# Optimization experiments

Hardware: AMD Instinct MI355X
Metric: run time of the kernel (lower is better)

## Reference

```python
import jax, jax.numpy as jnp
import numpy as np

N = 150000   # total supergraph nodes (entities+events+chains)
D = 128      # embed_size
H = 4        # attention heads
DH = D // H  # head dim
E = 300000   # edges per layer
L = 4        # layer_specs length
A = 8        # edge attr dim
T = 10       # num_edge_type
TIME_SCALE = 24.0
SLOPE = 0.2  # negative_slope


def setup_inputs() -> dict:
    key = jax.random.key(0)
    ks = jax.random.split(key, 16)
    nrm = lambda k, s, sc=1.0: jax.random.normal(k, s, dtype=jnp.float32) * sc
    return {
        'x': nrm(ks[0], (N, D), 0.1),
        'Wq': nrm(ks[1], (L, D, D), D ** -0.5),
        'Wk': nrm(ks[2], (L, D, D), D ** -0.5),
        'Wv': nrm(ks[3], (L, D, D), D ** -0.5),
        'Wskip': nrm(ks[4], (L, D, D), D ** -0.5),
        'Wa': nrm(ks[5], (L, A, D), 0.1),
        'time_w': nrm(ks[6], (D,)),
        'time_b': nrm(ks[7], (D,), 0.1),
        'dist_w': nrm(ks[8], (D,)),
        'dist_b': nrm(ks[9], (D,), 0.1),
        'type_table': nrm(ks[10], (T, D), 0.1),
        'bn_gamma': jnp.ones((L, D), jnp.float32),
        'bn_beta': jnp.zeros((L, D), jnp.float32),
        'beta': jnp.full((L,), 0.5, jnp.float32),
        'edge_attr': jax.random.uniform(ks[11], (L, E, A), dtype=jnp.float32),
        'edge_dt': jax.random.uniform(ks[12], (L, E), dtype=jnp.float32) * TIME_SCALE,
        'edge_ds': jax.random.uniform(ks[13], (L, E), dtype=jnp.float32) * 10.0,
        'edge_index': jax.random.randint(ks[14], (L, 2, E), 0, N),
        'edge_type': jax.random.randint(ks[15], (L, E), 0, T),
    }


def _layer(x, Wq, Wk, Wv, Wskip, Wa, time_w, time_b, dist_w, dist_b,
           type_table, gamma, bvec, beta, attr, dt, ds, ei, et):
    n = x.shape[0]
    src, dst = ei[0], ei[1]
    # continuous time / distance encoders: cos basis (TimeEncoder / 'time' DistanceEncoder)
    te = jnp.cos((dt / TIME_SCALE)[:, None] * time_w + time_b)   # [E,D]
    de = jnp.cos(ds[:, None] * dist_w + dist_b)                  # [E,D]
    # 'add' edge/time fusion: attr MLP + time + dist + edge-type embeddings
    edge_feat = attr @ Wa + te + de + type_table[et]             # [E,D]
    kv_in = x[src] + edge_feat                                   # gather + fuse
    q = (x @ Wq).reshape(n, H, DH)[dst]                          # [E,H,DH]
    k = (kv_in @ Wk).reshape(-1, H, DH)
    v = (kv_in @ Wv).reshape(-1, H, DH)
    logits = (q * k).sum(-1) * (DH ** -0.5)                      # [E,H]
    logits = jnp.where(logits >= 0, logits, SLOPE * logits)      # leaky_relu(negative_slope)
    # segment softmax over incoming edges of each destination node
    m = jax.ops.segment_max(logits, dst, num_segments=n)
    a = jnp.exp(logits - m[dst])
    denom = jax.ops.segment_sum(a, dst, num_segments=n)
    a = a / denom[dst]
    agg = jax.ops.segment_sum(a[..., None] * v, dst, num_segments=n).reshape(n, D)
    # beta-weighted residual (learn_beta) with skip projection
    out = beta * (x @ Wskip) + (1.0 - beta) * agg
    # BatchNorm1d (training-mode batch stats) + ReLU
    mu = out.mean(0)
    var = out.var(0)
    out = (out - mu) * jax.lax.rsqrt(var + 1e-5) * gamma + bvec
    return jax.nn.relu(out)


def reference(x, Wq, Wk, Wv, Wskip, Wa, time_w, time_b, dist_w, dist_b,
              type_table, bn_gamma, bn_beta, beta, edge_attr, edge_dt,
              edge_ds, edge_index, edge_type):
    for l in range(L):  # entity2event, event2event, event2chain (time filter), chain2chain
        x = _layer(x, Wq[l], Wk[l], Wv[l], Wskip[l], Wa[l],
                   time_w, time_b, dist_w, dist_b, type_table,
                   bn_gamma[l], bn_beta[l], beta[l],
                   edge_attr[l], edge_dt[l], edge_ds[l],
                   edge_index[l], edge_type[l])
    return x
```

## Files before the change

### kernel.cpp

```cpp
#include <hip/hip_runtime.h>

typedef unsigned int u32;
typedef unsigned short u16;
typedef short bf16x8 __attribute__((ext_vector_type(8)));
typedef float f32x4 __attribute__((ext_vector_type(4)));

#define N_NODES 150000
#define E_EDGES 300000
#define L_CNT   151552
#define ETILES  9375
#define NTILES  4688

__device__ __forceinline__ float blo(u32 u){ return __uint_as_float(u << 16); }
__device__ __forceinline__ float bhi(u32 u){ return __uint_as_float(u & 0xffff0000u); }
__device__ __forceinline__ float b2f(u16 h){ return __uint_as_float(((u32)h) << 16); }
__device__ __forceinline__ u16 f2bf(float f){
  u32 u = __float_as_uint(f);
  return (u16)((u + 0x7fffu + ((u >> 16) & 1u)) >> 16);
}
__device__ __forceinline__ u32 pack2(float a, float b){
  return (u32)f2bf(a) | ((u32)f2bf(b) << 16);
}

__device__ __forceinline__ f32x4 mfma16(bf16x8 a, bf16x8 b, f32x4 c){
  return __builtin_amdgcn_mfma_f32_16x16x32_bf16(a, b, c, 0, 0, 0);
}

__device__ __forceinline__ int opsw(int r, int k){ return (r * 128 + k) ^ ((r & 7) << 3); }
__device__ __forceinline__ int csw(int r, int n){ return (r * 128 + n) ^ (((r >> 2) & 3) << 3); }

__global__ __launch_bounds__(256)
void k_wt(const float* __restrict__ Wq, const float* __restrict__ Wk,
          const float* __restrict__ Wv, const float* __restrict__ Ws,
          u16* __restrict__ Wt)
{
  const int m = blockIdx.x;
  const float* src = (m < 4 ? Wq : m < 8 ? Wk : m < 12 ? Wv : Ws)
                     + (size_t)(m & 3) * 16384;
  u16* dst = Wt + (size_t)m * 16384;
  const int t = threadIdx.x;
  for (int i = 0; i < 16; ++i) {
    int idx = i * 256 + t;
    int n = idx >> 5;
    int k4 = (idx & 31) << 2;
    ushort4 o;
    o.x = f2bf(src[(k4 + 0) * 128 + n]);
    o.y = f2bf(src[(k4 + 1) * 128 + n]);
    o.z = f2bf(src[(k4 + 2) * 128 + n]);
    o.w = f2bf(src[(k4 + 3) * 128 + n]);
    *(ushort4*)(dst + n * 128 + k4) = o;
  }
}


__global__ __launch_bounds__(256)
void k_hist(const int* __restrict__ eidx, int* __restrict__ counts)
{
  const int l = blockIdx.y;
  const int e = blockIdx.x * 256 + threadIdx.x;
  if (e < E_EDGES) {
    int dst = eidx[(size_t)l * 2 * E_EDGES + E_EDGES + e];
    atomicAdd(&counts[(size_t)l * L_CNT + dst], 1);
  }
}

__global__ __launch_bounds__(256)
void k_scan1(const int* __restrict__ counts, int* __restrict__ rowptr,
             int* __restrict__ bsum)
{
  __shared__ int sh[256];
  const int b = blockIdx.x, l = blockIdx.y;
  const int t = threadIdx.x;
  const int* c = counts + (size_t)l * L_CNT + b * 2048;
  int* rp = rowptr + (size_t)l * L_CNT + b * 2048;
  int v[8]; int s = 0;
  #pragma unroll
  for (int j = 0; j < 8; ++j) { v[j] = c[t * 8 + j]; s += v[j]; }
  sh[t] = s; __syncthreads();
  for (int off = 1; off < 256; off <<= 1) {
    int x = (t >= off) ? sh[t - off] : 0;
    __syncthreads();
    sh[t] += x;
    __syncthreads();
  }
  int excl = (t == 0) ? 0 : sh[t - 1];
  if (t == 255) bsum[l * 128 + b] = sh[255];
  int run = excl;
  #pragma unroll
  for (int j = 0; j < 8; ++j) { rp[t * 8 + j] = run; run += v[j]; }
}

__global__ __launch_bounds__(128)
void k_scan2(int* __restrict__ bsum)
{
  __shared__ int sh[128];
  const int l = blockIdx.x, t = threadIdx.x;
  int v = (t < 74) ? bsum[l * 128 + t] : 0;
  sh[t] = v; __syncthreads();
  for (int off = 1; off < 128; off <<= 1) {
    int x = (t >= off) ? sh[t - off] : 0;
    __syncthreads();
    sh[t] += x;
    __syncthreads();
  }
  int excl = (t == 0) ? 0 : sh[t - 1];
  if (t < 74) bsum[l * 128 + t] = excl;
}

__global__ __launch_bounds__(256)
void k_scan3(int* __restrict__ rowptr, int* __restrict__ tmp,
             const int* __restrict__ bsum)
{
  const int l = blockIdx.y;
  const int q = blockIdx.x * 256 + threadIdx.x;
  int v = rowptr[(size_t)l * L_CNT + q] + bsum[l * 128 + (q >> 11)];
  rowptr[(size_t)l * L_CNT + q] = v;
  tmp[(size_t)l * L_CNT + q] = v;
}

__global__ __launch_bounds__(256)
void k_scatter(const int* __restrict__ srcP, const int* __restrict__ dstP,
               const int* __restrict__ etP, const float* __restrict__ dtP,
               const float* __restrict__ dsP, const float* __restrict__ attrP,
               int* __restrict__ tmpL, u32* __restrict__ meta)
{
  const int e = blockIdx.x * 256 + threadIdx.x;
  if (e < E_EDGES) {
    int dst = dstP[e];
    int pos = atomicAdd(&tmpL[dst], 1);
    int src = srcP[e];
    int et  = etP[e];
    float dtn = dtP[e] * (1.0f / 24.0f);
    float dsv = dsP[e];
    float4 aA = *(const float4*)(attrP + (size_t)e * 8);
    float4 aB = *(const float4*)(attrP + (size_t)e * 8 + 4);
    uint4 r0, r1;
    r0.x = (u32)src;
    r0.y = (u32)dst | ((u32)et << 20);
    r0.z = __float_as_uint(dtn);
    r0.w = __float_as_uint(dsv);
    r1.x = pack2(aA.x, aA.y); r1.y = pack2(aA.z, aA.w);
    r1.z = pack2(aB.x, aB.y); r1.w = pack2(aB.z, aB.w);
    u32* mp = meta + (size_t)pos * 8;
    *(uint4*)mp = r0;
    *(uint4*)(mp + 4) = r1;
  }
}

template<int XF32>
__global__ __launch_bounds__(256)
void k_kvin(const void* __restrict__ xg, const float* __restrict__ Wa,
            const float* __restrict__ tw, const float* __restrict__ tb,
            const float* __restrict__ dw, const float* __restrict__ db,
            const float* __restrict__ ttab, const u32* __restrict__ meta,
            u16* __restrict__ kvV)
{
  const int idx = blockIdx.x * 256 + threadIdx.x;
  const int e = idx >> 4;
  const int c8 = (idx & 15) << 3;
  const u32* mp = meta + (size_t)e * 8;
  uint4 m0 = *(const uint4*)mp;
  uint4 m1 = *(const uint4*)(mp + 4);
  const int src = (int)m0.x;
  const int et = (int)(m0.y >> 20);
  const float dtn = __uint_as_float(m0.z);
  const float dss = __uint_as_float(m0.w);
  float aa[8] = { blo(m1.x), bhi(m1.x), blo(m1.y), bhi(m1.y),
                  blo(m1.z), bhi(m1.z), blo(m1.w), bhi(m1.w) };
  const float4 twA = *(const float4*)(tw + c8);
  const float4 twB = *(const float4*)(tw + c8 + 4);
  const float4 tbA = *(const float4*)(tb + c8);
  const float4 tbB = *(const float4*)(tb + c8 + 4);
  const float4 dwA = *(const float4*)(dw + c8);
  const float4 dwB = *(const float4*)(dw + c8 + 4);
  const float4 dbA = *(const float4*)(db + c8);
  const float4 dbB = *(const float4*)(db + c8 + 4);
  const float4 ttA = *(const float4*)(ttab + et * 128 + c8);
  const float4 ttB = *(const float4*)(ttab + et * 128 + c8 + 4);
  float f[8];
  f[0] = __cosf(fmaf(dtn, twA.x, tbA.x)) + __cosf(fmaf(dss, dwA.x, dbA.x)) + ttA.x;
  f[1] = __cosf(fmaf(dtn, twA.y, tbA.y)) + __cosf(fmaf(dss, dwA.y, dbA.y)) + ttA.y;
  f[2] = __cosf(fmaf(dtn, twA.z, tbA.z)) + __cosf(fmaf(dss, dwA.z, dbA.z)) + ttA.z;
  f[3] = __cosf(fmaf(dtn, twA.w, tbA.w)) + __cosf(fmaf(dss, dwA.w, dbA.w)) + ttA.w;
  f[4] = __cosf(fmaf(dtn, twB.x, tbB.x)) + __cosf(fmaf(dss, dwB.x, dbB.x)) + ttB.x;
  f[5] = __cosf(fmaf(dtn, twB.y, tbB.y)) + __cosf(fmaf(dss, dwB.y, dbB.y)) + ttB.y;
  f[6] = __cosf(fmaf(dtn, twB.z, tbB.z)) + __cosf(fmaf(dss, dwB.z, dbB.z)) + ttB.z;
  f[7] = __cosf(fmaf(dtn, twB.w, tbB.w)) + __cosf(fmaf(dss, dwB.w, dbB.w)) + ttB.w;
  #pragma unroll
  for (int a = 0; a < 8; ++a) {
    float4 wA = *(const float4*)(Wa + a * 128 + c8);
    float4 wB = *(const float4*)(Wa + a * 128 + c8 + 4);
    f[0] = fmaf(aa[a], wA.x, f[0]);
    f[1] = fmaf(aa[a], wA.y, f[1]);
    f[2] = fmaf(aa[a], wA.z, f[2]);
    f[3] = fmaf(aa[a], wA.w, f[3]);
    f[4] = fmaf(aa[a], wB.x, f[4]);
    f[5] = fmaf(aa[a], wB.y, f[5]);
    f[6] = fmaf(aa[a], wB.z, f[6]);
    f[7] = fmaf(aa[a], wB.w, f[7]);
  }
  float xv[8];
  if (XF32) {
    float4 xA = *(const float4*)((const float*)xg + (size_t)src * 128 + c8);
    float4 xB = *(const float4*)((const float*)xg + (size_t)src * 128 + c8 + 4);
    xv[0] = xA.x; xv[1] = xA.y; xv[2] = xA.z; xv[3] = xA.w;
    xv[4] = xB.x; xv[5] = xB.y; xv[6] = xB.z; xv[7] = xB.w;
  } else {
    uint4 xr = *(const uint4*)((const u16*)xg + (size_t)src * 128 + c8);
    xv[0] = blo(xr.x); xv[1] = bhi(xr.x); xv[2] = blo(xr.y); xv[3] = bhi(xr.y);
    xv[4] = blo(xr.z); xv[5] = bhi(xr.z); xv[6] = blo(xr.w); xv[7] = bhi(xr.w);
  }
  uint4 o;
  o.x = pack2(xv[0] + f[0], xv[1] + f[1]);
  o.y = pack2(xv[2] + f[2], xv[3] + f[3]);
  o.z = pack2(xv[4] + f[4], xv[5] + f[5]);
  o.w = pack2(xv[6] + f[6], xv[7] + f[7]);
  *(uint4*)(kvV + (size_t)e * 128 + c8) = o;
}


template<int XF32>
__global__ __launch_bounds__(128, 2)
void gemm_qs(const void* __restrict__ xg, const u16* __restrict__ WtQ,
             const u16* __restrict__ WtS, u16* __restrict__ Qo,
             u16* __restrict__ So)
{
  __shared__ __align__(16) u16 As[4160];
  __shared__ __align__(16) u16 Bs[4160];
  const int t = threadIdx.x;
  const int w = t >> 6, lane = t & 63;
  const int lr = lane & 15, hi = lane >> 4;
  const int row0 = blockIdx.x * 32;
  const int nr = min(32, N_NODES - row0);
  const u16* Wt = w ? WtS : WtQ;
  u16* C = w ? So : Qo;

  bf16x8 wt[8][4];
  #pragma unroll
  for (int nb = 0; nb < 8; ++nb)
    #pragma unroll
    for (int ks = 0; ks < 4; ++ks)
      wt[nb][ks] = *(const bf16x8*)(Wt + (nb * 16 + lr) * 128 + ks * 32 + hi * 8);

  #pragma unroll
  for (int i = 0; i < 4; ++i) {
    int idx = i * 128 + t;
    int r = idx >> 4, c8 = (idx & 15) << 3;
    if (r < nr) {
      if (XF32) {
        float4 vA = *(const float4*)((const float*)xg + (size_t)(row0 + r) * 128 + c8);
        float4 vB = *(const float4*)((const float*)xg + (size_t)(row0 + r) * 128 + c8 + 4);
        uint4 o;
        o.x = pack2(vA.x, vA.y); o.y = pack2(vA.z, vA.w);
        o.z = pack2(vB.x, vB.y); o.w = pack2(vB.z, vB.w);
        *(uint4*)(As + opsw(r, c8)) = o;
      } else {
        uint4 v = *(const uint4*)((const u16*)xg + (size_t)(row0 + r) * 128 + c8);
        *(uint4*)(As + opsw(r, c8)) = v;
      }
    } else {
      *(uint4*)(As + opsw(r, c8)) = make_uint4(0, 0, 0, 0);
    }
  }
  __syncthreads();

  f32x4 acc[2][8];
  #pragma unroll
  for (int a = 0; a < 2; ++a)
    #pragma unroll
    for (int b = 0; b < 8; ++b) {
      acc[a][b][0] = 0.f; acc[a][b][1] = 0.f;
      acc[a][b][2] = 0.f; acc[a][b][3] = 0.f;
    }
  #pragma unroll
  for (int ks = 0; ks < 4; ++ks) {
    const int kb = ks * 32 + hi * 8;
    bf16x8 a0 = *(const bf16x8*)(As + opsw(lr, kb));
    bf16x8 a1 = *(const bf16x8*)(As + opsw(16 + lr, kb));
    #pragma unroll
    for (int nb = 0; nb < 8; ++nb) {
      acc[0][nb] = mfma16(a0, wt[nb][ks], acc[0][nb]);
      acc[1][nb] = mfma16(a1, wt[nb][ks], acc[1][nb]);
    }
  }
  __syncthreads();

  u16* Cs = w ? Bs : As;
  const int g4 = hi << 2;
  #pragma unroll
  for (int mt = 0; mt < 2; ++mt)
    #pragma unroll
    for (int nt = 0; nt < 8; ++nt)
      #pragma unroll
      for (int j = 0; j < 4; ++j)
        Cs[csw(mt * 16 + g4 + j, nt * 16 + lr)] = f2bf(acc[mt][nt][j]);
  #pragma unroll
  for (int i = 0; i < 8; ++i) {
    int idx = i * 64 + lane;
    int r = idx >> 4, n8 = (idx & 15) << 3;
    if (r < nr) {
      uint4 v = *(const uint4*)(Cs + csw(r, n8));
      *(uint4*)(C + (size_t)(row0 + r) * 128 + n8) = v;
    }
  }
}


__global__ __launch_bounds__(128, 2)
void edge_kv(const u16* __restrict__ WtK, const u16* __restrict__ WtV,
             const u32* __restrict__ meta, const u16* __restrict__ Qb,
             u16* __restrict__ kvV, float* __restrict__ logits)
{
  __shared__ __align__(16) u16 KVs[4160];
  __shared__ __align__(16) u16 Qs[4160];
  __shared__ int dstSh[32];
  const int t = threadIdx.x;
  const int w = t >> 6, lane = t & 63;
  const int lr = lane & 15, hi = lane >> 4;
  const int e0 = blockIdx.x * 32;
  const u16* Wt = w ? WtV : WtK;

  bf16x8 wt[8][4];
  #pragma unroll
  for (int nb = 0; nb < 8; ++nb)
    #pragma unroll
    for (int ks = 0; ks < 4; ++ks)
      wt[nb][ks] = *(const bf16x8*)(Wt + (nb * 16 + lr) * 128 + ks * 32 + hi * 8);

  if (w == 0) {
    #pragma unroll
    for (int i = 0; i < 8; ++i) {
      int idx = i * 64 + lane;
      int r = idx >> 4, c8 = (idx & 15) << 3;
      uint4 v = *(const uint4*)(kvV + (size_t)(e0 + r) * 128 + c8);
      *(uint4*)(KVs + opsw(r, c8)) = v;
    }
  } else {
    if (lane < 32)
      dstSh[lane] = (int)(meta[(size_t)(e0 + lane) * 8 + 1] & 0xFFFFFu);
    #pragma unroll
    for (int i = 0; i < 8; ++i) {
      int idx = i * 64 + lane;
      int r = idx >> 4, c8 = (idx & 15) << 3;
      int qrow = dstSh[r];
      uint4 qv = *(const uint4*)(Qb + (size_t)qrow * 128 + c8);
      *(uint4*)(Qs + opsw(r, c8)) = qv;
    }
  }
  __syncthreads();

  if (w == 0) {
    #pragma unroll
    for (int eb = 0; eb < 2; ++eb) {
      f32x4 kacc[8];
      #pragma unroll
      for (int b = 0; b < 8; ++b) {
        kacc[b][0] = 0.f; kacc[b][1] = 0.f; kacc[b][2] = 0.f; kacc[b][3] = 0.f;
      }
      #pragma unroll
      for (int ks = 0; ks < 4; ++ks) {
        bf16x8 ef = *(const bf16x8*)(KVs + opsw(eb * 16 + lr, ks * 32 + hi * 8));
        #pragma unroll
        for (int nb = 0; nb < 8; ++nb)
          kacc[nb] = mfma16(wt[nb][ks], ef, kacc[nb]);
      }
      const int el = eb * 16 + lr;
      float hs[4] = {0.f, 0.f, 0.f, 0.f};
      #pragma unroll
      for (int nb = 0; nb < 8; ++nb) {
        ushort4 q = *(const ushort4*)(Qs + opsw(el, nb * 16 + hi * 4));
        hs[nb >> 1] += b2f(q.x) * kacc[nb][0] + b2f(q.y) * kacc[nb][1]
                     + b2f(q.z) * kacc[nb][2] + b2f(q.w) * kacc[nb][3];
      }
      #pragma unroll
      for (int h = 0; h < 4; ++h) {
        hs[h] += __shfl_xor(hs[h], 16, 64);
        hs[h] += __shfl_xor(hs[h], 32, 64);
        hs[h] *= 0.17677669529663687f;
        hs[h] = (hs[h] >= 0.f) ? hs[h] : 0.2f * hs[h];
      }
      if (lane < 16)
        *(float4*)(logits + (size_t)(e0 + el) * 4) = make_float4(hs[0], hs[1], hs[2], hs[3]);
    }
    __syncthreads();
  } else {
    f32x4 vacc[2][8];
    #pragma unroll
    for (int a = 0; a < 2; ++a)
      #pragma unroll
      for (int b = 0; b < 8; ++b) {
        vacc[a][b][0] = 0.f; vacc[a][b][1] = 0.f;
        vacc[a][b][2] = 0.f; vacc[a][b][3] = 0.f;
      }
    #pragma unroll
    for (int ks = 0; ks < 4; ++ks) {
      const int kb = ks * 32 + hi * 8;
      bf16x8 a0 = *(const bf16x8*)(KVs + opsw(lr, kb));
      bf16x8 a1 = *(const bf16x8*)(KVs + opsw(16 + lr, kb));
      #pragma unroll
      for (int nb = 0; nb < 8; ++nb) {
        vacc[0][nb] = mfma16(a0, wt[nb][ks], vacc[0][nb]);
        vacc[1][nb] = mfma16(a1, wt[nb][ks], vacc[1][nb]);
      }
    }
    __syncthreads();
    const int g4 = hi << 2;
    #pragma unroll
    for (int mt = 0; mt < 2; ++mt)
      #pragma unroll
      for (int nt = 0; nt < 8; ++nt)
        #pragma unroll
        for (int j = 0; j < 4; ++j)
          Qs[csw(mt * 16 + g4 + j, nt * 16 + lr)] = f2bf(vacc[mt][nt][j]);
    #pragma unroll
    for (int i = 0; i < 8; ++i) {
      int idx = i * 64 + lane;
      int r = idx >> 4, n8 = (idx & 15) << 3;
      uint4 v = *(const uint4*)(Qs + csw(r, n8));
      *(uint4*)(kvV + (size_t)(e0 + r) * 128 + n8) = v;
    }
  }
}

__global__ __launch_bounds__(256)
void node_agg(const u16* __restrict__ Vs, const float* __restrict__ logits,
              const int* __restrict__ rowptr, const u16* __restrict__ S,
              const float* __restrict__ betaP, float* __restrict__ pre,
              float* __restrict__ colsum, float* __restrict__ colsumsq)
{
  __shared__ float red[1024];
  const int t = threadIdx.x;
  const int g = t >> 5;
  const int lane = t & 31;
  const int d0 = lane * 4;
  const int h = lane >> 3;
  const float beta = *betaP;
  const float omb = 1.f - beta;
  float s4[4] = {0.f, 0.f, 0.f, 0.f};
  float q4[4] = {0.f, 0.f, 0.f, 0.f};
  for (int rep = 0; rep < 16; ++rep) {
    int n = blockIdx.x * 128 + rep * 8 + g;
    if (n < N_NODES) {
      int rs = rowptr[n], re = rowptr[n + 1];
      float m = -1e30f;
      for (int i = rs; i < re; ++i)
        m = fmaxf(m, logits[(size_t)i * 4 + h]);
      float den = 0.f;
      float a0 = 0.f, a1 = 0.f, a2 = 0.f, a3 = 0.f;
      for (int i = rs; i < re; ++i) {
        float wgt = __expf(logits[(size_t)i * 4 + h] - m);
        den += wgt;
        ushort4 v = *(const ushort4*)(Vs + (size_t)i * 128 + d0);
        a0 = fmaf(wgt, b2f(v.x), a0);
        a1 = fmaf(wgt, b2f(v.y), a1);
        a2 = fmaf(wgt, b2f(v.z), a2);
        a3 = fmaf(wgt, b2f(v.w), a3);
      }
      float inv = (den > 0.f) ? (omb / den) : 0.f;
      ushort4 sv = *(const ushort4*)(S + (size_t)n * 128 + d0);
      float p0 = fmaf(beta, b2f(sv.x), a0 * inv);
      float p1 = fmaf(beta, b2f(sv.y), a1 * inv);
      float p2 = fmaf(beta, b2f(sv.z), a2 * inv);
      float p3 = fmaf(beta, b2f(sv.w), a3 * inv);
      *(float4*)(pre + (size_t)n * 128 + d0) = make_float4(p0, p1, p2, p3);
      s4[0] += p0; s4[1] += p1; s4[2] += p2; s4[3] += p3;
      q4[0] += p0 * p0; q4[1] += p1 * p1; q4[2] += p2 * p2; q4[3] += p3 * p3;
    }
  }
  *(float4*)(&red[g * 128 + d0]) = make_float4(s4[0], s4[1], s4[2], s4[3]);
  __syncthreads();
  if (t < 128) {
    float tot = 0.f;
    #pragma unroll
    for (int gg = 0; gg < 8; ++gg) tot += red[gg * 128 + t];
    atomicAdd(&colsum[t], tot);
  }
  __syncthreads();
  *(float4*)(&red[g * 128 + d0]) = make_float4(q4[0], q4[1], q4[2], q4[3]);
  __syncthreads();
  if (t < 128) {
    float tot = 0.f;
    #pragma unroll
    for (int gg = 0; gg < 8; ++gg) tot += red[gg * 128 + t];
    atomicAdd(&colsumsq[t], tot);
  }
}

template<int LAST>
__global__ __launch_bounds__(256)
void bn_apply(const float* __restrict__ pre, const float* __restrict__ colsum,
              const float* __restrict__ colsumsq, const float* __restrict__ gamma,
              const float* __restrict__ bvec, u16* __restrict__ outbf,
              float* __restrict__ outf)
{
  const int idx = blockIdx.x * 256 + threadIdx.x;
  const int n = idx >> 5;
  const int d0 = (idx & 31) * 4;
  const float invN = 1.f / 150000.f;
  float4 p = *(const float4*)(pre + (size_t)n * 128 + d0);
  float4 cs = *(const float4*)(colsum + d0);
  float4 cq = *(const float4*)(colsumsq + d0);
  float4 gm = *(const float4*)(gamma + d0);
  float4 bv = *(const float4*)(bvec + d0);
  float mu, var, y;
  mu = cs.x * invN; var = cq.x * invN - mu * mu;
  y = (p.x - mu) * rsqrtf(var + 1e-5f) * gm.x + bv.x; p.x = fmaxf(y, 0.f);
  mu = cs.y * invN; var = cq.y * invN - mu * mu;
  y = (p.y - mu) * rsqrtf(var + 1e-5f) * gm.y + bv.y; p.y = fmaxf(y, 0.f);
  mu = cs.z * invN; var = cq.z * invN - mu * mu;
  y = (p.z - mu) * rsqrtf(var + 1e-5f) * gm.z + bv.z; p.z = fmaxf(y, 0.f);
  mu = cs.w * invN; var = cq.w * invN - mu * mu;
  y = (p.w - mu) * rsqrtf(var + 1e-5f) * gm.w + bv.w; p.w = fmaxf(y, 0.f);
  if (LAST) {
    *(float4*)(outf + (size_t)n * 128 + d0) = p;
  } else {
    ushort4 o;
    o.x = f2bf(p.x); o.y = f2bf(p.y); o.z = f2bf(p.z); o.w = f2bf(p.w);
    *(ushort4*)(outbf + (size_t)n * 128 + d0) = o;
  }
}

extern "C" void kernel_launch(void* const* d_in, const int* in_sizes, int n_in,
                              void* d_out, int out_size, void* d_ws, size_t ws_size,
                              hipStream_t stream)
{
  const float* x0    = (const float*)d_in[0];
  const float* Wq    = (const float*)d_in[1];
  const float* Wk    = (const float*)d_in[2];
  const float* Wv    = (const float*)d_in[3];
  const float* Wsk   = (const float*)d_in[4];
  const float* Wa    = (const float*)d_in[5];
  const float* tw    = (const float*)d_in[6];
  const float* tb    = (const float*)d_in[7];
  const float* dw    = (const float*)d_in[8];
  const float* db    = (const float*)d_in[9];
  const float* ttab  = (const float*)d_in[10];
  const float* gam   = (const float*)d_in[11];
  const float* bet   = (const float*)d_in[12];
  const float* betaP = (const float*)d_in[13];
  const float* attr  = (const float*)d_in[14];
  const float* dt    = (const float*)d_in[15];
  const float* dsv   = (const float*)d_in[16];
  const int*   eidx  = (const int*)d_in[17];
  const int*   etyp  = (const int*)d_in[18];

  char* p = (char*)d_ws;
  u16* xbf  = (u16*)p;       p += 38400000;
  u16* Q    = (u16*)p;       p += 38400000;
  u16* S    = (u16*)p;       p += 38400000;
  u16* kvV  = (u16*)p;       p += 76800000;
  float* logits = (float*)p; p += 4800000;
  int* rowptr = (int*)p;     p += 4 * L_CNT * 4;
  int* tmp    = (int*)p;     p += 4 * L_CNT * 4;
  int* bsum   = (int*)p;     p += 4 * 128 * 4;
  float* colsum   = (float*)p; p += 512;
  float* colsumsq = (float*)p; p += 512;
  u16* Wt = (u16*)p;         p += 16 * 16384 * 2;
  u32* meta = (u32*)p;       p += (size_t)E_EDGES * 32;

  float* pre = (float*)d_out;

  k_wt<<<16, 256, 0, stream>>>(Wq, Wk, Wv, Wsk, Wt);
  hipMemsetAsync(tmp, 0, 4 * L_CNT * 4, stream);
  k_hist<<<dim3(1172, 4), 256, 0, stream>>>(eidx, tmp);
  k_scan1<<<dim3(74, 4), 256, 0, stream>>>(tmp, rowptr, bsum);
  k_scan2<<<4, 128, 0, stream>>>(bsum);
  k_scan3<<<dim3(592, 4), 256, 0, stream>>>(rowptr, tmp, bsum);

  for (int l = 0; l < 4; ++l) {
    const int* srcA = eidx + (size_t)l * 600000;
    const int* dstA = srcA + 300000;
    const int* rpl = rowptr + (size_t)l * L_CNT;
    const u16* WtQl = Wt + (size_t)l * 16384;
    const u16* WtKl = Wt + (size_t)(4 + l) * 16384;
    const u16* WtVl = Wt + (size_t)(8 + l) * 16384;
    const u16* WtSl = Wt + (size_t)(12 + l) * 16384;
    const float* Wal = Wa + (size_t)l * 1024;

    k_scatter<<<1172, 256, 0, stream>>>(
        srcA, dstA, etyp + (size_t)l * 300000, dt + (size_t)l * 300000,
        dsv + (size_t)l * 300000, attr + (size_t)l * 2400000,
        tmp + (size_t)l * L_CNT, meta);

    hipMemsetAsync(colsum, 0, 1024, stream);

    if (l == 0) {
      k_kvin<1><<<18750, 256, 0, stream>>>((const void*)x0, Wal, tw, tb, dw, db,
                                           ttab, meta, kvV);
      gemm_qs<1><<<NTILES, 128, 0, stream>>>((const void*)x0, WtQl, WtSl, Q, S);
    } else {
      k_kvin<0><<<18750, 256, 0, stream>>>((const void*)xbf, Wal, tw, tb, dw, db,
                                           ttab, meta, kvV);
      gemm_qs<0><<<NTILES, 128, 0, stream>>>((const void*)xbf, WtQl, WtSl, Q, S);
    }

    edge_kv<<<ETILES, 128, 0, stream>>>(WtKl, WtVl, meta, Q, kvV, logits);

    node_agg<<<1172, 256, 0, stream>>>(kvV, logits, rpl, S, betaP + l,
                                       pre, colsum, colsumsq);

    if (l < 3)
      bn_apply<0><<<18750, 256, 0, stream>>>(pre, colsum, colsumsq,
                                             gam + (size_t)l * 128,
                                             bet + (size_t)l * 128, xbf, nullptr);
    else
      bn_apply<1><<<18750, 256, 0, stream>>>(pre, colsum, colsumsq,
                                             gam + (size_t)l * 128,
                                             bet + (size_t)l * 128,
                                             nullptr, (float*)d_out);
  }
}
```

Before: 1.503 ms.

## Fold BatchNorm+ReLU into next layer's consumers and process two tiles per GEMM block

For the first three layers, node_agg now writes the pre-norm output as bf16 into xbf. A tiny bn_stats kernel computes per-column scale and shift, and k_kvin and gemm_qs apply the BN affine and ReLU on load. This removes the separate bn_apply pass and its fp32 write and read of the full node tensor, at the cost of rounding to bf16 before normalization. gemm_qs and edge_kv also loop over two 32-row tiles per block, halving the grid and reusing the register-resident weight fragments across both tiles.

```diff
diff --git a/kernel.cpp b/kernel.cpp
--- a/kernel.cpp
+++ b/kernel.cpp
@@ -147,13 +147,27 @@
   }
 }
 
-template<int XF32>
+__global__ __launch_bounds__(128)
+void bn_stats(const float* __restrict__ colsum, const float* __restrict__ colsumsq,
+              const float* __restrict__ gamma, const float* __restrict__ bvec,
+              float* __restrict__ scsh)
+{
+  const int d = threadIdx.x;
+  const float invN = 1.f / 150000.f;
+  float mu = colsum[d] * invN;
+  float var = colsumsq[d] * invN - mu * mu;
+  float sc = gamma[d] * rsqrtf(var + 1e-5f);
+  scsh[d] = sc;
+  scsh[128 + d] = bvec[d] - mu * sc;
+}
+
+template<int XF32, int BN>
 __global__ __launch_bounds__(256)
 void k_kvin(const void* __restrict__ xg, const float* __restrict__ Wa,
             const float* __restrict__ tw, const float* __restrict__ tb,
             const float* __restrict__ dw, const float* __restrict__ db,
             const float* __restrict__ ttab, const u32* __restrict__ meta,
-            u16* __restrict__ kvV)
+            const float* __restrict__ scsh, u16* __restrict__ kvV)
 {
   const int idx = blockIdx.x * 256 + threadIdx.x;
   const int e = idx >> 4;
@@ -210,6 +224,20 @@
     xv[0] = blo(xr.x); xv[1] = bhi(xr.x); xv[2] = blo(xr.y); xv[3] = bhi(xr.y);
     xv[4] = blo(xr.z); xv[5] = bhi(xr.z); xv[6] = blo(xr.w); xv[7] = bhi(xr.w);
   }
+  if (BN) {
+    float4 scA = *(const float4*)(scsh + c8);
+    float4 scB = *(const float4*)(scsh + c8 + 4);
+    float4 shA = *(const float4*)(scsh + 128 + c8);
+    float4 shB = *(const float4*)(scsh + 128 + c8 + 4);
+    xv[0] = fmaxf(fmaf(xv[0], scA.x, shA.x), 0.f);
+    xv[1] = fmaxf(fmaf(xv[1], scA.y, shA.y), 0.f);
+    xv[2] = fmaxf(fmaf(xv[2], scA.z, shA.z), 0.f);
+    xv[3] = fmaxf(fmaf(xv[3], scA.w, shA.w), 0.f);
+    xv[4] = fmaxf(fmaf(xv[4], scB.x, shB.x), 0.f);
+    xv[5] = fmaxf(fmaf(xv[5], scB.y, shB.y), 0.f);
+    xv[6] = fmaxf(fmaf(xv[6], scB.z, shB.z), 0.f);
+    xv[7] = fmaxf(fmaf(xv[7], scB.w, shB.w), 0.f);
+  }
   uint4 o;
   o.x = pack2(xv[0] + f[0], xv[1] + f[1]);
   o.y = pack2(xv[2] + f[2], xv[3] + f[3]);
@@ -219,19 +247,17 @@
 }
 
 
-template<int XF32>
+template<int XF32, int BN>
 __global__ __launch_bounds__(128, 2)
 void gemm_qs(const void* __restrict__ xg, const u16* __restrict__ WtQ,
-             const u16* __restrict__ WtS, u16* __restrict__ Qo,
-             u16* __restrict__ So)
+             const u16* __restrict__ WtS, const float* __restrict__ scsh,
+             u16* __restrict__ Qo, u16* __restrict__ So)
 {
   __shared__ __align__(16) u16 As[4160];
   __shared__ __align__(16) u16 Bs[4160];
   const int t = threadIdx.x;
   const int w = t >> 6, lane = t & 63;
   const int lr = lane & 15, hi = lane >> 4;
-  const int row0 = blockIdx.x * 32;
-  const int nr = min(32, N_NODES - row0);
   const u16* Wt = w ? WtS : WtQ;
   u16* C = w ? So : Qo;
 
@@ -242,66 +268,90 @@
     for (int ks = 0; ks < 4; ++ks)
       wt[nb][ks] = *(const bf16x8*)(Wt + (nb * 16 + lr) * 128 + ks * 32 + hi * 8);
 
-  #pragma unroll
-  for (int i = 0; i < 4; ++i) {
-    int idx = i * 128 + t;
-    int r = idx >> 4, c8 = (idx & 15) << 3;
-    if (r < nr) {
-      if (XF32) {
-        float4 vA = *(const float4*)((const float*)xg + (size_t)(row0 + r) * 128 + c8);
-        float4 vB = *(const float4*)((const float*)xg + (size_t)(row0 + r) * 128 + c8 + 4);
-        uint4 o;
-        o.x = pack2(vA.x, vA.y); o.y = pack2(vA.z, vA.w);
-        o.z = pack2(vB.x, vB.y); o.w = pack2(vB.z, vB.w);
-        *(uint4*)(As + opsw(r, c8)) = o;
+  for (int tt = 0; tt < 2; ++tt) {
+    const int tile = blockIdx.x * 2 + tt;
+    const int row0 = tile * 32;
+    if (row0 >= N_NODES) break;
+    const int nr = min(32, N_NODES - row0);
+
+    #pragma unroll
+    for (int i = 0; i < 4; ++i) {
+      int idx = i * 128 + t;
+      int r = idx >> 4, c8 = (idx & 15) << 3;
+      if (r < nr) {
+        if (XF32) {
+          float4 vA = *(const float4*)((const float*)xg + (size_t)(row0 + r) * 128 + c8);
+          float4 vB = *(const float4*)((const float*)xg + (size_t)(row0 + r) * 128 + c8 + 4);
+          uint4 o;
+          o.x = pack2(vA.x, vA.y); o.y = pack2(vA.z, vA.w);
+          o.z = pack2(vB.x, vB.y); o.w = pack2(vB.z, vB.w);
+          *(uint4*)(As + opsw(r, c8)) = o;
+        } else {
+          uint4 v = *(const uint4*)((const u16*)xg + (size_t)(row0 + r) * 128 + c8);
+          if (BN) {
+            float4 scA = *(const float4*)(scsh + c8);
+            float4 scB = *(const float4*)(scsh + c8 + 4);
+            float4 shA = *(const float4*)(scsh + 128 + c8);
+            float4 shB = *(const float4*)(scsh + 128 + c8 + 4);
+            float e0v = fmaxf(fmaf(blo(v.x), scA.x, shA.x), 0.f);
+            float e1v = fmaxf(fmaf(bhi(v.x), scA.y, shA.y), 0.f);
+            float e2v = fmaxf(fmaf(blo(v.y), scA.z, shA.z), 0.f);
+            float e3v = fmaxf(fmaf(bhi(v.y), scA.w, shA.w), 0.f);
+            float e4v = fmaxf(fmaf(blo(v.z), scB.x, shB.x), 0.f);
+            float e5v = fmaxf(fmaf(bhi(v.z), scB.y, shB.y), 0.f);
+            float e6v = fmaxf(fmaf(blo(v.w), scB.z, shB.z), 0.f);
+            float e7v = fmaxf(fmaf(bhi(v.w), scB.w, shB.w), 0.f);
+            v.x = pack2(e0v, e1v); v.y = pack2(e2v, e3v);
+            v.z = pack2(e4v, e5v); v.w = pack2(e6v, e7v);
+          }
+          *(uint4*)(As + opsw(r, c8)) = v;
+        }
       } else {
-        uint4 v = *(const uint4*)((const u16*)xg + (size_t)(row0 + r) * 128 + c8);
-        *(uint4*)(As + opsw(r, c8)) = v;
-      }
-    } else {
-      *(uint4*)(As + opsw(r, c8)) = make_uint4(0, 0, 0, 0);
-    }
-  }
-  __syncthreads();
-
-  f32x4 acc[2][8];
-  #pragma unroll
-  for (int a = 0; a < 2; ++a)
-    #pragma unroll
-    for (int b = 0; b < 8; ++b) {
-      acc[a][b][0] = 0.f; acc[a][b][1] = 0.f;
-      acc[a][b][2] = 0.f; acc[a][b][3] = 0.f;
-    }
-  #pragma unroll
-  for (int ks = 0; ks < 4; ++ks) {
-    const int kb = ks * 32 + hi * 8;
-    bf16x8 a0 = *(const bf16x8*)(As + opsw(lr, kb));
-    bf16x8 a1 = *(const bf16x8*)(As + opsw(16 + lr, kb));
-    #pragma unroll
-    for (int nb = 0; nb < 8; ++nb) {
-      acc[0][nb] = mfma16(a0, wt[nb][ks], acc[0][nb]);
-      acc[1][nb] = mfma16(a1, wt[nb][ks], acc[1][nb]);
-    }
-  }
-  __syncthreads();
-
-  u16* Cs = w ? Bs : As;
-  const int g4 = hi << 2;
-  #pragma unroll
-  for (int mt = 0; mt < 2; ++mt)
-    #pragma unroll
-    for (int nt = 0; nt < 8; ++nt)
-      #pragma unroll
-      for (int j = 0; j < 4; ++j)
-        Cs[csw(mt * 16 + g4 + j, nt * 16 + lr)] = f2bf(acc[mt][nt][j]);
-  #pragma unroll
-  for (int i = 0; i < 8; ++i) {
-    int idx = i * 64 + lane;
-    int r = idx >> 4, n8 = (idx & 15) << 3;
-    if (r < nr) {
-      uint4 v = *(const uint4*)(Cs + csw(r, n8));
-      *(uint4*)(C + (size_t)(row0 + r) * 128 + n8) = v;
-    }
+        *(uint4*)(As + opsw(r, c8)) = make_uint4(0, 0, 0, 0);
+      }
+    }
+    __syncthreads();
+
+    f32x4 acc[2][8];
+    #pragma unroll
+    for (int a = 0; a < 2; ++a)
+      #pragma unroll
+      for (int b = 0; b < 8; ++b) {
+        acc[a][b][0] = 0.f; acc[a][b][1] = 0.f;
+        acc[a][b][2] = 0.f; acc[a][b][3] = 0.f;
+      }
+    #pragma unroll
+    for (int ks = 0; ks < 4; ++ks) {
+      const int kb = ks * 32 + hi * 8;
+      bf16x8 a0 = *(const bf16x8*)(As + opsw(lr, kb));
+      bf16x8 a1 = *(const bf16x8*)(As + opsw(16 + lr, kb));
+      #pragma unroll
+      for (int nb = 0; nb < 8; ++nb) {
+        acc[0][nb] = mfma16(a0, wt[nb][ks], acc[0][nb]);
+        acc[1][nb] = mfma16(a1, wt[nb][ks], acc[1][nb]);
+      }
+    }
+    __syncthreads();
+
+    u16* Cs = w ? Bs : As;
+    const int g4 = hi << 2;
+    #pragma unroll
+    for (int mt = 0; mt < 2; ++mt)
+      #pragma unroll
+      for (int nt = 0; nt < 8; ++nt)
+        #pragma unroll
+        for (int j = 0; j < 4; ++j)
+          Cs[csw(mt * 16 + g4 + j, nt * 16 + lr)] = f2bf(acc[mt][nt][j]);
+    #pragma unroll
+    for (int i = 0; i < 8; ++i) {
+      int idx = i * 64 + lane;
+      int r = idx >> 4, n8 = (idx & 15) << 3;
+      if (r < nr) {
+        uint4 v = *(const uint4*)(Cs + csw(r, n8));
+        *(uint4*)(C + (size_t)(row0 + r) * 128 + n8) = v;
+      }
+    }
+    __syncthreads();
   }
 }
 
@@ -317,7 +367,6 @@
   const int t = threadIdx.x;
   const int w = t >> 6, lane = t & 63;
   const int lr = lane & 15, hi = lane >> 4;
-  const int e0 = blockIdx.x * 32;
   const u16* Wt = w ? WtV : WtK;
 
   bf16x8 wt[8][4];
@@ -327,106 +376,115 @@
     for (int ks = 0; ks < 4; ++ks)
       wt[nb][ks] = *(const bf16x8*)(Wt + (nb * 16 + lr) * 128 + ks * 32 + hi * 8);
 
-  if (w == 0) {
-    #pragma unroll
-    for (int i = 0; i < 8; ++i) {
-      int idx = i * 64 + lane;
-      int r = idx >> 4, c8 = (idx & 15) << 3;
-      uint4 v = *(const uint4*)(kvV + (size_t)(e0 + r) * 128 + c8);
-      *(uint4*)(KVs + opsw(r, c8)) = v;
-    }
-  } else {
-    if (lane < 32)
-      dstSh[lane] = (int)(meta[(size_t)(e0 + lane) * 8 + 1] & 0xFFFFFu);
-    #pragma unroll
-    for (int i = 0; i < 8; ++i) {
-      int idx = i * 64 + lane;
-      int r = idx >> 4, c8 = (idx & 15) << 3;
-      int qrow = dstSh[r];
-      uint4 qv = *(const uint4*)(Qb + (size_t)qrow * 128 + c8);
-      *(uint4*)(Qs + opsw(r, c8)) = qv;
-    }
-  }
-  __syncthreads();
-
-  if (w == 0) {
-    #pragma unroll
-    for (int eb = 0; eb < 2; ++eb) {
-      f32x4 kacc[8];
-      #pragma unroll
-      for (int b = 0; b < 8; ++b) {
-        kacc[b][0] = 0.f; kacc[b][1] = 0.f; kacc[b][2] = 0.f; kacc[b][3] = 0.f;
-      }
+  for (int tt = 0; tt < 2; ++tt) {
+    const int e0 = (blockIdx.x * 2 + tt) * 32;
+    if (e0 >= E_EDGES) break;
+
+    if (w == 0) {
+      #pragma unroll
+      for (int i = 0; i < 8; ++i) {
+        int idx = i * 64 + lane;
+        int r = idx >> 4, c8 = (idx & 15) << 3;
+        uint4 v = *(const uint4*)(kvV + (size_t)(e0 + r) * 128 + c8);
+        *(uint4*)(KVs + opsw(r, c8)) = v;
+      }
+    } else {
+      if (lane < 32)
+        dstSh[lane] = (int)(meta[(size_t)(e0 + lane) * 8 + 1] & 0xFFFFFu);
+      #pragma unroll
+      for (int i = 0; i < 8; ++i) {
+        int idx = i * 64 + lane;
+        int r = idx >> 4, c8 = (idx & 15) << 3;
+        int qrow = dstSh[r];
+        uint4 qv = *(const uint4*)(Qb + (size_t)qrow * 128 + c8);
+        *(uint4*)(Qs + opsw(r, c8)) = qv;
+      }
+    }
+    __syncthreads();
+
+    if (w == 0) {
+      #pragma unroll
+      for (int eb = 0; eb < 2; ++eb) {
+        f32x4 kacc[8];
+        #pragma unroll
+        for (int b = 0; b < 8; ++b) {
+          kacc[b][0] = 0.f; kacc[b][1] = 0.f; kacc[b][2] = 0.f; kacc[b][3] = 0.f;
+        }
+        #pragma unroll
+        for (int ks = 0; ks < 4; ++ks) {
+          bf16x8 ef = *(const bf16x8*)(KVs + opsw(eb * 16 + lr, ks * 32 + hi * 8));
+          #pragma unroll
+          for (int nb = 0; nb < 8; ++nb)
+            kacc[nb] = mfma16(wt[nb][ks], ef, kacc[nb]);
+        }
+        const int el = eb * 16 + lr;
+        float hs[4] = {0.f, 0.f, 0.f, 0.f};
+        #pragma unroll
+        for (int nb = 0; nb < 8; ++nb) {
+          ushort4 q = *(const ushort4*)(Qs + opsw(el, nb * 16 + hi * 4));
+          hs[nb >> 1] += b2f(q.x) * kacc[nb][0] + b2f(q.y) * kacc[nb][1]
+                       + b2f(q.z) * kacc[nb][2] + b2f(q.w) * kacc[nb][3];
+        }
+        #pragma unroll
+        for (int h = 0; h < 4; ++h) {
+          hs[h] += __shfl_xor(hs[h], 16, 64);
+          hs[h] += __shfl_xor(hs[h], 32, 64);
+          hs[h] *= 0.17677669529663687f;
+          hs[h] = (hs[h] >= 0.f) ? hs[h] : 0.2f * hs[h];
+        }
+        if (lane < 16)
+          *(float4*)(logits + (size_t)(e0 + el) * 4) = make_float4(hs[0], hs[1], hs[2], hs[3]);
+      }
+      __syncthreads();
+      __syncthreads();
+    } else {
+      f32x4 vacc[2][8];
+      #pragma unroll
+      for (int a = 0; a < 2; ++a)
+        #pragma unroll
+        for (int b = 0; b < 8; ++b) {
+          vacc[a][b][0] = 0.f; vacc[a][b][1] = 0.f;
+          vacc[a][b][2] = 0.f; vacc[a][b][3] = 0.f;
+        }
       #pragma unroll
       for (int ks = 0; ks < 4; ++ks) {
-        bf16x8 ef = *(const bf16x8*)(KVs + opsw(eb * 16 + lr, ks * 32 + hi * 8));
-        #pragma unroll
-        for (int nb = 0; nb < 8; ++nb)
-          kacc[nb] = mfma16(wt[nb][ks], ef, kacc[nb]);
-      }
-      const int el = eb * 16 + lr;
-      float hs[4] = {0.f, 0.f, 0.f, 0.f};
-      #pragma unroll
-      for (int nb = 0; nb < 8; ++nb) {
-        ushort4 q = *(const ushort4*)(Qs + opsw(el, nb * 16 + hi * 4));
-        hs[nb >> 1] += b2f(q.x) * kacc[nb][0] + b2f(q.y) * kacc[nb][1]
-                     + b2f(q.z) * kacc[nb][2] + b2f(q.w) * kacc[nb][3];
-      }
-      #pragma unroll
-      for (int h = 0; h < 4; ++h) {
-        hs[h] += __shfl_xor(hs[h], 16, 64);
-        hs[h] += __shfl_xor(hs[h], 32, 64);
-        hs[h] *= 0.17677669529663687f;
-        hs[h] = (hs[h] >= 0.f) ? hs[h] : 0.2f * hs[h];
-      }
-      if (lane < 16)
-        *(float4*)(logits + (size_t)(e0 + el) * 4) = make_float4(hs[0], hs[1], hs[2], hs[3]);
-    }
-    __syncthreads();
-  } else {
-    f32x4 vacc[2][8];
-    #pragma unroll
-    for (int a = 0; a < 2; ++a)
-      #pragma unroll
-      for (int b = 0; b < 8; ++b) {
-        vacc[a][b][0] = 0.f; vacc[a][b][1] = 0.f;
-        vacc[a][b][2] = 0.f; vacc[a][b][3] = 0.f;
-      }
-    #pragma unroll
-    for (int ks = 0; ks < 4; ++ks) {
-      const int kb = ks * 32 + hi * 8;
-      bf16x8 a0 = *(const bf16x8*)(KVs + opsw(lr, kb));
-      bf16x8 a1 = *(const bf16x8*)(KVs + opsw(16 + lr, kb));
-      #pragma unroll
-      for (int nb = 0; nb < 8; ++nb) {
-        vacc[0][nb] = mfma16(a0, wt[nb][ks], vacc[0][nb]);
-        vacc[1][nb] = mfma16(a1, wt[nb][ks], vacc[1][nb]);
-      }
-    }
-    __syncthreads();
-    const int g4 = hi << 2;
-    #pragma unroll
-    for (int mt = 0; mt < 2; ++mt)
-      #pragma unroll
-      for (int nt = 0; nt < 8; ++nt)
-        #pragma unroll
-        for (int j = 0; j < 4; ++j)
-          Qs[csw(mt * 16 + g4 + j, nt * 16 + lr)] = f2bf(vacc[mt][nt][j]);
-    #pragma unroll
-    for (int i = 0; i < 8; ++i) {
-      int idx = i * 64 + lane;
-      int r = idx >> 4, n8 = (idx & 15) << 3;
-      uint4 v = *(const uint4*)(Qs + csw(r, n8));
-      *(uint4*)(kvV + (size_t)(e0 + r) * 128 + n8) = v;
-    }
-  }
-}
-
+        const int kb = ks * 32 + hi * 8;
+        bf16x8 a0 = *(const bf16x8*)(KVs + opsw(lr, kb));
+        bf16x8 a1 = *(const bf16x8*)(KVs + opsw(16 + lr, kb));
+        #pragma unroll
+        for (int nb = 0; nb < 8; ++nb) {
+          vacc[0][nb] = mfma16(a0, wt[nb][ks], vacc[0][nb]);
+          vacc[1][nb] = mfma16(a1, wt[nb][ks], vacc[1][nb]);
+        }
+      }
+      __syncthreads();
+      const int g4 = hi << 2;
+      #pragma unroll
+      for (int mt = 0; mt < 2; ++mt)
+        #pragma unroll
+        for (int nt = 0; nt < 8; ++nt)
+          #pragma unroll
+          for (int j = 0; j < 4; ++j)
+            Qs[csw(mt * 16 + g4 + j, nt * 16 + lr)] = f2bf(vacc[mt][nt][j]);
+      #pragma unroll
+      for (int i = 0; i < 8; ++i) {
+        int idx = i * 64 + lane;
+        int r = idx >> 4, n8 = (idx & 15) << 3;
+        uint4 v = *(const uint4*)(Qs + csw(r, n8));
+        *(uint4*)(kvV + (size_t)(e0 + r) * 128 + n8) = v;
+      }
+      __syncthreads();
+    }
+  }
+}
+
+template<int PREBF16>
 __global__ __launch_bounds__(256)
 void node_agg(const u16* __restrict__ Vs, const float* __restrict__ logits,
               const int* __restrict__ rowptr, const u16* __restrict__ S,
               const float* __restrict__ betaP, float* __restrict__ pre,
-              float* __restrict__ colsum, float* __restrict__ colsumsq)
+              u16* __restrict__ preb, float* __restrict__ colsum,
+              float* __restrict__ colsumsq)
 {
   __shared__ float red[1024];
   const int t = threadIdx.x;
@@ -462,7 +520,13 @@
       float p1 = fmaf(beta, b2f(sv.y), a1 * inv);
       float p2 = fmaf(beta, b2f(sv.z), a2 * inv);
       float p3 = fmaf(beta, b2f(sv.w), a3 * inv);
-      *(float4*)(pre + (size_t)n * 128 + d0) = make_float4(p0, p1, p2, p3);
+      if (PREBF16) {
+        ushort4 o;
+        o.x = f2bf(p0); o.y = f2bf(p1); o.z = f2bf(p2); o.w = f2bf(p3);
+        *(ushort4*)(preb + (size_t)n * 128 + d0) = o;
+      } else {
+        *(float4*)(pre + (size_t)n * 128 + d0) = make_float4(p0, p1, p2, p3);
+      }
       s4[0] += p0; s4[1] += p1; s4[2] += p2; s4[3] += p3;
       q4[0] += p0 * p0; q4[1] += p1 * p1; q4[2] += p2 * p2; q4[3] += p3 * p3;
     }
@@ -486,12 +550,10 @@
   }
 }
 
-template<int LAST>
 __global__ __launch_bounds__(256)
 void bn_apply(const float* __restrict__ pre, const float* __restrict__ colsum,
               const float* __restrict__ colsumsq, const float* __restrict__ gamma,
-              const float* __restrict__ bvec, u16* __restrict__ outbf,
-              float* __restrict__ outf)
+              const float* __restrict__ bvec, float* __restrict__ outf)
 {
   const int idx = blockIdx.x * 256 + threadIdx.x;
   const int n = idx >> 5;
@@ -511,13 +573,7 @@
   y = (p.z - mu) * rsqrtf(var + 1e-5f) * gm.z + bv.z; p.z = fmaxf(y, 0.f);
   mu = cs.w * invN; var = cq.w * invN - mu * mu;
   y = (p.w - mu) * rsqrtf(var + 1e-5f) * gm.w + bv.w; p.w = fmaxf(y, 0.f);
-  if (LAST) {
-    *(float4*)(outf + (size_t)n * 128 + d0) = p;
-  } else {
-    ushort4 o;
-    o.x = f2bf(p.x); o.y = f2bf(p.y); o.z = f2bf(p.z); o.w = f2bf(p.w);
-    *(ushort4*)(outbf + (size_t)n * 128 + d0) = o;
-  }
+  *(float4*)(outf + (size_t)n * 128 + d0) = p;
 }
 
 extern "C" void kernel_launch(void* const* d_in, const int* in_sizes, int n_in,
@@ -555,6 +611,7 @@
   int* bsum   = (int*)p;     p += 4 * 128 * 4;
   float* colsum   = (float*)p; p += 512;
   float* colsumsq = (float*)p; p += 512;
+  float* scsh     = (float*)p; p += 1024;
   u16* Wt = (u16*)p;         p += 16 * 16384 * 2;
   u32* meta = (u32*)p;       p += (size_t)E_EDGES * 32;
 
@@ -585,28 +642,28 @@
     hipMemsetAsync(colsum, 0, 1024, stream);
 
     if (l == 0) {
-      k_kvin<1><<<18750, 256, 0, stream>>>((const void*)x0, Wal, tw, tb, dw, db,
-                                           ttab, meta, kvV);
-      gemm_qs<1><<<NTILES, 128, 0, stream>>>((const void*)x0, WtQl, WtSl, Q, S);
+      k_kvin<1, 0><<<18750, 256, 0, stream>>>((const void*)x0, Wal, tw, tb, dw, db,
+                                              ttab, meta, scsh, kvV);
+      gemm_qs<1, 0><<<2344, 128, 0, stream>>>((const void*)x0, WtQl, WtSl, scsh, Q, S);
     } else {
-      k_kvin<0><<<18750, 256, 0, stream>>>((const void*)xbf, Wal, tw, tb, dw, db,
-                                           ttab, meta, kvV);
-      gemm_qs<0><<<NTILES, 128, 0, stream>>>((const void*)xbf, WtQl, WtSl, Q, S);
-    }
-
-    edge_kv<<<ETILES, 128, 0, stream>>>(WtKl, WtVl, meta, Q, kvV, logits);
-
-    node_agg<<<1172, 256, 0, stream>>>(kvV, logits, rpl, S, betaP + l,
-                                       pre, colsum, colsumsq);
-
-    if (l < 3)
-      bn_apply<0><<<18750, 256, 0, stream>>>(pre, colsum, colsumsq,
-                                             gam + (size_t)l * 128,
-                                             bet + (size_t)l * 128, xbf, nullptr);
-    else
-      bn_apply<1><<<18750, 256, 0, stream>>>(pre, colsum, colsumsq,
-                                             gam + (size_t)l * 128,
-                                             bet + (size_t)l * 128,
-                                             nullptr, (float*)d_out);
-  }
-}
+      k_kvin<0, 1><<<18750, 256, 0, stream>>>((const void*)xbf, Wal, tw, tb, dw, db,
+                                              ttab, meta, scsh, kvV);
+      gemm_qs<0, 1><<<2344, 128, 0, stream>>>((const void*)xbf, WtQl, WtSl, scsh, Q, S);
+    }
+
+    edge_kv<<<4688, 128, 0, stream>>>(WtKl, WtVl, meta, Q, kvV, logits);
+
+    if (l < 3) {
+      node_agg<1><<<1172, 256, 0, stream>>>(kvV, logits, rpl, S, betaP + l,
+                                            nullptr, xbf, colsum, colsumsq);
+      bn_stats<<<1, 128, 0, stream>>>(colsum, colsumsq, gam + (size_t)l * 128,
+                                      bet + (size_t)l * 128, scsh);
+    } else {
+      node_agg<0><<<1172, 256, 0, stream>>>(kvV, logits, rpl, S, betaP + l,
+                                            pre, nullptr, colsum, colsumsq);
+      bn_apply<<<18750, 256, 0, stream>>>(pre, colsum, colsumsq,
+                                          gam + (size_t)l * 128,
+                                          bet + (size_t)l * 128, (float*)d_out);
+    }
+  }
+}
```

Result: slower. 1.969 ms (+31.0%).
